# Kernel optimization log

Hardware: AMD Instinct MI355X
Metric: run time of the kernel (lower is better)

Reference implementation:

```python
import jax, jax.numpy as jnp
import numpy as np

H = 4  # num_heads


def transformer_conv(x, src, dst, wq, bq, wk, bk, wv, bv, ws, bs):
    # PyG TransformerConv, concat=False, root_weight=True, eval mode (no dropout).
    N = x.shape[0]
    C = wq.shape[1] // H  # per-head channels
    q = (x @ wq + bq).reshape(N, H, C)
    k = (x @ wk + bk).reshape(N, H, C)
    v = (x @ wv + bv).reshape(N, H, C)
    # per-edge attention logits: query at dst, key at src
    logits = (q[dst] * k[src]).sum(-1) / jnp.sqrt(jnp.asarray(C, x.dtype))  # [E,H]
    # scatter-softmax over incoming edges of each destination node
    m = jax.lax.stop_gradient(jax.ops.segment_max(logits, dst, num_segments=N))
    m = jnp.where(jnp.isfinite(m), m, jnp.zeros_like(m))
    e = jnp.exp(logits - m[dst])
    denom = jax.ops.segment_sum(e, dst, num_segments=N)
    alpha = e / (denom[dst] + 1e-16)  # [E,H]
    out = jax.ops.segment_sum(alpha[:, :, None] * v[src], dst, num_segments=N)  # [N,H,C]
    return out.mean(axis=1) + x @ ws + bs  # head-average + skip


def setup_inputs() -> dict:
    key = jax.random.key(0)
    ks = jax.random.split(key, 16)
    N, E, D, HID, OUT = 50000, 800000, 128, 32, 40
    s = 0.05
    inp = {
        "x": jax.random.normal(ks[0], (N, D), jnp.float32),
        "edge_index": jax.random.randint(ks[1], (2, E), 0, N, jnp.int64),
        "wq1": jax.random.normal(ks[2], (D, H * HID), jnp.float32) * s,
        "bq1": jnp.zeros((H * HID,), jnp.float32),
        "wk1": jax.random.normal(ks[3], (D, H * HID), jnp.float32) * s,
        "bk1": jnp.zeros((H * HID,), jnp.float32),
        "wv1": jax.random.normal(ks[4], (D, H * HID), jnp.float32) * s,
        "bv1": jnp.zeros((H * HID,), jnp.float32),
        "ws1": jax.random.normal(ks[5], (D, HID), jnp.float32) * s,
        "bs1": jnp.zeros((HID,), jnp.float32),
        "wq2": jax.random.normal(ks[6], (HID, H * HID), jnp.float32) * s,
        "bq2": jnp.zeros((H * HID,), jnp.float32),
        "wk2": jax.random.normal(ks[7], (HID, H * HID), jnp.float32) * s,
        "bk2": jnp.zeros((H * HID,), jnp.float32),
        "wv2": jax.random.normal(ks[8], (HID, H * HID), jnp.float32) * s,
        "bv2": jnp.zeros((H * HID,), jnp.float32),
        "ws2": jax.random.normal(ks[9], (HID, HID), jnp.float32) * s,
        "bs2": jnp.zeros((HID,), jnp.float32),
        "wc": jax.random.normal(ks[10], (HID, OUT), jnp.float32) * s,
        "bc": jnp.zeros((OUT,), jnp.float32),
    }
    return inp


def reference(x, edge_index, wq1, bq1, wk1, bk1, wv1, bv1, ws1, bs1,
              wq2, bq2, wk2, bk2, wv2, bv2, ws2, bs2, wc, bc):
    src, dst = edge_index[0], edge_index[1]
    h = jax.nn.relu(transformer_conv(x, src, dst, wq1, bq1, wk1, bk1, wv1, bv1, ws1, bs1))
    h = jax.nn.relu(transformer_conv(h, src, dst, wq2, bq2, wk2, bk2, wv2, bv2, ws2, bs2))
    return h @ wc + bc
```

## Files before the change

### kernel.cpp

```cpp
#include <hip/hip_runtime.h>
#include <hip/hip_bf16.h>

typedef __attribute__((ext_vector_type(8))) short short8;
typedef __attribute__((ext_vector_type(4))) float floatx4;
typedef __attribute__((ext_vector_type(4))) unsigned short ushort4v;

__device__ inline unsigned short f2bf(float x) {
    unsigned int u = __float_as_uint(x);
    u += 0x7FFFu + ((u >> 16) & 1u);
    return (unsigned short)(u >> 16);
}
__device__ inline float bf2f(unsigned short h) {
    return __uint_as_float(((unsigned int)h) << 16);
}
__device__ inline float blo(unsigned int u) { return __uint_as_float(u << 16); }
__device__ inline float bhi(unsigned int u) { return __uint_as_float(u & 0xFFFF0000u); }

#if defined(__has_builtin)
#if __has_builtin(__builtin_amdgcn_exp2f)
#define EXP2F(x) __builtin_amdgcn_exp2f(x)
#else
#define EXP2F(x) exp2f(x)
#endif
#if __has_builtin(__builtin_amdgcn_update_dpp)
#define HAVE_DPP 1
#endif
#else
#define EXP2F(x) exp2f(x)
#endif

#ifdef HAVE_DPP
template <int CTRL>
__device__ __forceinline__ float dppadd(float x) {
    int s = __builtin_amdgcn_update_dpp(0, __float_as_int(x), CTRL, 0xf, 0xf, true);
    return x + __int_as_float(s);
}
__device__ __forceinline__ float red8(float x) {
    x = dppadd<0xB1>(x);
    x = dppadd<0x4E>(x);
    x = dppadd<0x141>(x);
    return x;
}
__device__ __forceinline__ float xor8add(float x) {
    return dppadd<0x128>(x);
}
#else
__device__ __forceinline__ float red8(float x) {
    x += __shfl_xor(x, 1); x += __shfl_xor(x, 2); x += __shfl_xor(x, 4);
    return x;
}
__device__ __forceinline__ float xor8add(float x) { return x + __shfl_xor(x, 8); }
#endif

template <bool B> struct BC { static constexpr bool value = B; };

__global__ __launch_bounds__(256) void hist_kernel(
    const int* __restrict__ dst, int* __restrict__ deg, int E)
{
    int e = blockIdx.x * blockDim.x + threadIdx.x;
    if (e < E) atomicAdd(&deg[dst[e]], 1);
}

__global__ __launch_bounds__(256) void scan_part(
    const int* __restrict__ deg, int* __restrict__ bsum, int N)
{
    __shared__ int ws[4];
    const int base = blockIdx.x * 1024;
    const int tid = threadIdx.x, lane = tid & 63, w = tid >> 6;
    int s = 0;
#pragma unroll
    for (int j = 0; j < 4; j++) {
        int i = base + j * 256 + tid;
        if (i < N) s += deg[i];
    }
#pragma unroll
    for (int off = 1; off < 64; off <<= 1) s += __shfl_xor(s, off, 64);
    if (lane == 0) ws[w] = s;
    __syncthreads();
    if (tid == 0) bsum[blockIdx.x] = ws[0] + ws[1] + ws[2] + ws[3];
}

__global__ __launch_bounds__(64) void scan_tops(
    const int* __restrict__ bsum, int* __restrict__ boff,
    int* __restrict__ rowptr, int nb, int N)
{
    int lane = threadIdx.x;
    int v = (lane < nb) ? bsum[lane] : 0;
    int inc = v;
#pragma unroll
    for (int off = 1; off < 64; off <<= 1) {
        int t = __shfl_up(inc, off, 64);
        if (lane >= off) inc += t;
    }
    if (lane < nb) boff[lane] = inc - v;
    if (lane == 63) rowptr[N] = inc;
}

__global__ __launch_bounds__(256) void scan_final(
    const int* __restrict__ deg, const int* __restrict__ boff,
    int* __restrict__ rowptr, int* __restrict__ cursor, int N)
{
    __shared__ int woff[4];
    const int base = blockIdx.x * 1024;
    const int tid = threadIdx.x, lane = tid & 63, w = tid >> 6;
    const int i0 = base + tid * 4;
    int v0 = (i0     < N) ? deg[i0]     : 0;
    int v1 = (i0 + 1 < N) ? deg[i0 + 1] : 0;
    int v2 = (i0 + 2 < N) ? deg[i0 + 2] : 0;
    int v3 = (i0 + 3 < N) ? deg[i0 + 3] : 0;
    int ts = v0 + v1 + v2 + v3;
    int inc = ts;
#pragma unroll
    for (int off = 1; off < 64; off <<= 1) {
        int t = __shfl_up(inc, off, 64);
        if (lane >= off) inc += t;
    }
    if (lane == 63) woff[w] = inc;
    __syncthreads();
    int wpre = 0;
    if (w > 0) wpre += woff[0];
    if (w > 1) wpre += woff[1];
    if (w > 2) wpre += woff[2];
    int exc = boff[blockIdx.x] + wpre + inc - ts;
    int p0 = exc, p1 = exc + v0, p2 = p1 + v1, p3 = p2 + v2;
    if (i0     < N) { rowptr[i0]     = p0; cursor[i0]     = p0; }
    if (i0 + 1 < N) { rowptr[i0 + 1] = p1; cursor[i0 + 1] = p1; }
    if (i0 + 2 < N) { rowptr[i0 + 2] = p2; cursor[i0 + 2] = p2; }
    if (i0 + 3 < N) { rowptr[i0 + 3] = p3; cursor[i0 + 3] = p3; }
}

__global__ __launch_bounds__(256) void fill_kernel(
    const int* __restrict__ src, const int* __restrict__ dst,
    int* __restrict__ cursor, int* __restrict__ perm, int E)
{
    int e = blockIdx.x * blockDim.x + threadIdx.x;
    if (e >= E) return;
    int pos = atomicAdd(&cursor[dst[e]], 1);
    perm[pos] = src[e];
}

__global__ __launch_bounds__(128) void wprep_all(
    const float* __restrict__ wq1, const float* __restrict__ bq1,
    const float* __restrict__ wk1, const float* __restrict__ bk1,
    const float* __restrict__ wv1, const float* __restrict__ bv1,
    const float* __restrict__ ws1, const float* __restrict__ bs1,
    const float* __restrict__ wq2, const float* __restrict__ bq2,
    const float* __restrict__ wk2, const float* __restrict__ bk2,
    const float* __restrict__ wv2, const float* __restrict__ bv2,
    const float* __restrict__ ws2, const float* __restrict__ bs2,
    unsigned short* __restrict__ wt1h, unsigned short* __restrict__ wt1l,
    float* __restrict__ bias1,
    unsigned short* __restrict__ wt2h, unsigned short* __restrict__ wt2l,
    float* __restrict__ bias2,
    int* __restrict__ deg, int* __restrict__ perm, int N, int E)
{
    const int t = threadIdx.x;
    {
        int gid = blockIdx.x * 128 + t;
        if (gid < N) deg[gid] = 0;
        else if (gid < N + 48) perm[E + (gid - N)] = 0;
    }
    const int layer = (blockIdx.x >= 416) ? 1 : 0;
    const int c = blockIdx.x - layer * 416;
    const int L = layer ? 32 : 128;
    if (t >= L) return;
    const float* w; const float* b; int cc, ncols;
    if (c < 384) {
        int m = c >> 7; cc = c & 127; ncols = 128;
        if (layer == 0) {
            w = (m == 0) ? wq1 : ((m == 1) ? wk1 : wv1);
            b = (m == 0) ? bq1 : ((m == 1) ? bk1 : bv1);
        } else {
            w = (m == 0) ? wq2 : ((m == 1) ? wk2 : wv2);
            b = (m == 0) ? bq2 : ((m == 1) ? bk2 : bv2);
        }
    } else {
        cc = c - 384; ncols = 32;
        w = layer ? ws2 : ws1; b = layer ? bs2 : bs1;
    }
    unsigned short* wh = layer ? wt2h : wt1h;
    unsigned short* wl = layer ? wt2l : wt1l;
    float* bias = layer ? bias2 : bias1;
    const float QSCL = 0.17677669529663687f * 1.4426950408889634f;
    const float f = (c < 128) ? QSCL : 1.0f;
    float val = w[t * ncols + cc] * f;
    unsigned short h = f2bf(val);
    wh[c * L + t] = h;
    wl[c * L + t] = f2bf(val - bf2f(h));
    if (t == 0) bias[c] = b[cc] * f;
}

template <int L>
__global__ __launch_bounds__(512) void proj_mfma(
    const float* __restrict__ xin,
    const unsigned short* __restrict__ wt_hi,
    const unsigned short* __restrict__ wt_lo,
    const float* __restrict__ bias,
    float* __restrict__ q, unsigned short* __restrict__ kvp,
    float* __restrict__ skip, int N)
{
    constexpr int LP = L + 8;
    constexpr int KS = L / 32;
    constexpr int ELEMS = 32 * (L / 4);
    constexpr int SI = (ELEMS + 511) / 512;
    __shared__ unsigned short xh[2][32 * LP];
    __shared__ unsigned short xl[2][32 * LP];
    __shared__ float scr[8][32 * 36];
    const int tid = threadIdx.x, lane = tid & 63, w = tid >> 6;
    const int li = lane & 15, quad = lane >> 4;
    const int slot = __builtin_amdgcn_readfirstlane(blockIdx.y * 8 + w);
    const bool hasT = slot < 13;

    int t0 = 24, t1 = 25;
    if (slot < 4)       { t0 = slot * 2; t1 = t0 + 1; }
    else if (slot < 12) { t0 = 4 + slot; t1 = 12 + slot; }

    short8 Ah[2][KS], Al[2][KS];
    float bias_r[2][4];
    if (hasT) {
#pragma unroll
        for (int ti = 0; ti < 2; ti++) {
            int tt = ti ? t1 : t0;
#pragma unroll
            for (int ks = 0; ks < KS; ks++) {
                long off = (long)(tt * 16 + li) * L + ks * 32 + quad * 8;
                Ah[ti][ks] = *(const short8*)(wt_hi + off);
                Al[ti][ks] = *(const short8*)(wt_lo + off);
            }
#pragma unroll
            for (int r = 0; r < 4; r++)
                bias_r[ti][r] = bias[tt * 16 + quad * 4 + r];
        }
    }

    const int nb0 = blockIdx.x * 256;
    float* myscr = scr[w];
    unsigned int* su = (unsigned int*)myscr;

    float4 xv[SI];
    auto issue_loads = [&](int c) {
#pragma unroll
        for (int s = 0; s < SI; s++) {
            int f = s * 512 + tid;
            if (f < ELEMS) {
                int row = f / (L / 4), c4 = (f - row * (L / 4)) * 4;
                int n = nb0 + c * 32 + row;
                xv[s] = (n < N) ? *(const float4*)(xin + (long)n * L + c4)
                                : make_float4(0.f, 0.f, 0.f, 0.f);
            }
        }
    };
    auto cvt_store = [&](int buf) {
#pragma unroll
        for (int s = 0; s < SI; s++) {
            int f = s * 512 + tid;
            if (f < ELEMS) {
                int row = f / (L / 4), c4 = (f - row * (L / 4)) * 4;
                unsigned short h0 = f2bf(xv[s].x), h1 = f2bf(xv[s].y),
                               h2 = f2bf(xv[s].z), h3 = f2bf(xv[s].w);
                ushort4v hs = {h0, h1, h2, h3};
                ushort4v ls = {f2bf(xv[s].x - bf2f(h0)), f2bf(xv[s].y - bf2f(h1)),
                               f2bf(xv[s].z - bf2f(h2)), f2bf(xv[s].w - bf2f(h3))};
                *(ushort4v*)(xh[buf] + row * LP + c4) = hs;
                *(ushort4v*)(xl[buf] + row * LP + c4) = ls;
            }
        }
    };

    issue_loads(0);
    cvt_store(0);
    __syncthreads();

    for (int c = 0; c < 8; c++) {
        if (c < 7) issue_loads(c + 1);
        const int n0c = nb0 + c * 32;
        if (hasT) {
            const int buf = c & 1;
#pragma unroll
            for (int half = 0; half < 2; half++) {
                short8 Bh[KS], Bl[KS];
#pragma unroll
                for (int ks = 0; ks < KS; ks++) {
                    int off = (half * 16 + li) * LP + ks * 32 + quad * 8;
                    Bh[ks] = *(const short8*)(xh[buf] + off);
                    Bl[ks] = *(const short8*)(xl[buf] + off);
                }
                floatx4 accv[2];
#pragma unroll
                for (int ti = 0; ti < 2; ti++) {
                    floatx4 acc = {0.f, 0.f, 0.f, 0.f};
#pragma unroll
                    for (int ks = 0; ks < KS; ks++) {
                        acc = __builtin_amdgcn_mfma_f32_16x16x32_bf16(Ah[ti][ks], Bh[ks], acc, 0, 0, 0);
                        acc = __builtin_amdgcn_mfma_f32_16x16x32_bf16(Ah[ti][ks], Bl[ks], acc, 0, 0, 0);
                        acc = __builtin_amdgcn_mfma_f32_16x16x32_bf16(Al[ti][ks], Bh[ks], acc, 0, 0, 0);
                    }
#pragma unroll
                    for (int r = 0; r < 4; r++) acc[r] += bias_r[ti][r];
                    accv[ti] = acc;
                }
                const int row = half * 16 + li;
                if (slot < 4 || slot == 12) {
                    *(floatx4*)(myscr + row * 36 + quad * 4)      = accv[0];
                    *(floatx4*)(myscr + row * 36 + 16 + quad * 4) = accv[1];
                } else {
                    unsigned int k01 = (unsigned int)f2bf(accv[0][0]) | ((unsigned int)f2bf(accv[0][1]) << 16);
                    unsigned int k23 = (unsigned int)f2bf(accv[0][2]) | ((unsigned int)f2bf(accv[0][3]) << 16);
                    unsigned int v01 = (unsigned int)f2bf(accv[1][0]) | ((unsigned int)f2bf(accv[1][1]) << 16);
                    unsigned int v23 = (unsigned int)f2bf(accv[1][2]) | ((unsigned int)f2bf(accv[1][3]) << 16);
                    uint4 pk = make_uint4(k01, v01, k23, v23);
                    *(uint4*)(su + row * 20 + quad * 4) = pk;
                }
            }
            if (slot < 4) {
#pragma unroll
                for (int it = 0; it < 4; it++) {
                    int idx = it * 64 + lane;
                    int nl = idx >> 3, seg = idx & 7;
                    int node = n0c + nl;
                    if (node < N) {
                        floatx4 vv = *(floatx4*)(myscr + nl * 36 + seg * 4);
                        *(floatx4*)(q + (long)node * 128 + slot * 32 + seg * 4) = vv;
                    }
                }
            } else if (slot == 12) {
#pragma unroll
                for (int it = 0; it < 4; it++) {
                    int idx = it * 64 + lane;
                    int nl = idx >> 3, seg = idx & 7;
                    int node = n0c + nl;
                    if (node < N) {
                        floatx4 vv = *(floatx4*)(myscr + nl * 36 + seg * 4);
                        *(floatx4*)(skip + (long)node * 32 + seg * 4) = vv;
                    }
                }
            } else {
                const int i = slot - 4;
#pragma unroll
                for (int it = 0; it < 2; it++) {
                    int idx = it * 64 + lane;
                    int nl = idx >> 2, part = idx & 3;
                    int node = n0c + nl;
                    if (node < N) {
                        uint4 vv = *(uint4*)(su + nl * 20 + part * 4);
                        *(uint4*)((unsigned int*)(kvp + (long)node * 256) + i * 16 + part * 4) = vv;
                    }
                }
            }
        }
        __syncthreads();
        if (c < 7) cvt_store((c + 1) & 1);
        __syncthreads();
    }
}

template <bool FUSE_CLS>
__global__ __launch_bounds__(256) void attn_kernel(
    const float* __restrict__ q, const unsigned short* __restrict__ kvp,
    const int* __restrict__ rowptr, const int* __restrict__ perm,
    const float* __restrict__ skip, float* __restrict__ h,
    const float* __restrict__ wc, const float* __restrict__ bc,
    float* __restrict__ out, int N, int E)
{
    __shared__ float hrow[4][32];
    const int tid = threadIdx.x;
    const int wid = (blockIdx.x * 256 + tid) >> 6;
    const int wv = (tid >> 6) & 3;
    const int lane = tid & 63;
    if (wid >= N) return;
    const int d = __builtin_amdgcn_readfirstlane(wid);
    const int eh = lane >> 5;
    const int sl = lane & 31;
    const int hh = sl >> 3;
    const int g  = sl & 7;
    const unsigned dby = (unsigned)(hh * 64 + g * 8) * 2u;
    const char* __restrict__ kvb = (const char*)kvp;
    const float4 q4 = *(const float4*)(q + (long)d * 128 + hh * 32 + g * 4);

    const int beg = rowptr[d], end = rowptr[d + 1];
    const int n = end - beg;
    const int na = (n + 1) >> 1;
    const int nmin = n - na;
    const int my_off = beg + (eh ? na : 0);
    const int my_cnt = eh ? nmin : na;
    const int* __restrict__ pp = perm + my_off;

    float den = 0.f;
    float o0 = 0.f, o1 = 0.f, o2 = 0.f, o3 = 0.f;

    auto kvld = [&](int s) -> uint4 {
        return *(const uint4*)(kvb + ((((unsigned)s) << 9) + dby));
    };

    uint4 A0, A1, A2, A3, B0, B1, B2, B3, C0, C1, C2, C3;
    int PA0, PA1, PA2, PA3, PB0, PB1, PB2, PB3, PC0, PC1, PC2, PC3;
    {
        int i0 = pp[0], i1 = pp[1], i2  = pp[2],  i3  = pp[3];
        int i4 = pp[4], i5 = pp[5], i6  = pp[6],  i7  = pp[7];
        int i8 = pp[8], i9 = pp[9], i10 = pp[10], i11 = pp[11];
        PA0 = pp[12]; PA1 = pp[13]; PA2 = pp[14]; PA3 = pp[15];
        PB0 = pp[16]; PB1 = pp[17]; PB2 = pp[18]; PB3 = pp[19];
        PC0 = pp[20]; PC1 = pp[21]; PC2 = pp[22]; PC3 = pp[23];
        A0 = kvld(i0); A1 = kvld(i1); A2 = kvld(i2);  A3 = kvld(i3);
        B0 = kvld(i4); B1 = kvld(i5); B2 = kvld(i6);  B3 = kvld(i7);
        C0 = kvld(i8); C1 = kvld(i9); C2 = kvld(i10); C3 = kvld(i11);
    }

    auto grp = [&](const uint4& G0, const uint4& G1, const uint4& G2,
                   const uint4& G3, int jb, auto mc) {
        constexpr bool MASKED = decltype(mc)::value;
        float p0 = q4.x * blo(G0.x) + q4.y * bhi(G0.x) + q4.z * blo(G0.z) + q4.w * bhi(G0.z);
        float p1 = q4.x * blo(G1.x) + q4.y * bhi(G1.x) + q4.z * blo(G1.z) + q4.w * bhi(G1.z);
        float p2 = q4.x * blo(G2.x) + q4.y * bhi(G2.x) + q4.z * blo(G2.z) + q4.w * bhi(G2.z);
        float p3 = q4.x * blo(G3.x) + q4.y * bhi(G3.x) + q4.z * blo(G3.z) + q4.w * bhi(G3.z);
        p0 = red8(p0); p1 = red8(p1); p2 = red8(p2); p3 = red8(p3);
        p0 = fminf(p0, 60.f); p1 = fminf(p1, 60.f);
        p2 = fminf(p2, 60.f); p3 = fminf(p3, 60.f);
        if (MASKED) {
            p0 = (jb + 0 < my_cnt) ? p0 : -INFINITY;
            p1 = (jb + 1 < my_cnt) ? p1 : -INFINITY;
            p2 = (jb + 2 < my_cnt) ? p2 : -INFINITY;
            p3 = (jb + 3 < my_cnt) ? p3 : -INFINITY;
        }
        const float w0 = EXP2F(p0), w1 = EXP2F(p1);
        const float w2 = EXP2F(p2), w3 = EXP2F(p3);
        den += (w0 + w1) + (w2 + w3);
        o0 += w0 * blo(G0.y) + w1 * blo(G1.y) + w2 * blo(G2.y) + w3 * blo(G3.y);
        o1 += w0 * bhi(G0.y) + w1 * bhi(G1.y) + w2 * bhi(G2.y) + w3 * bhi(G3.y);
        o2 += w0 * blo(G0.w) + w1 * blo(G1.w) + w2 * blo(G2.w) + w3 * blo(G3.w);
        o3 += w0 * bhi(G0.w) + w1 * bhi(G1.w) + w2 * bhi(G2.w) + w3 * bhi(G3.w);
    };

    int j = 0;
    for (; j + 12 <= nmin; j += 12) {
        grp(A0, A1, A2, A3, j, BC<false>{});
        A0 = kvld(PA0); A1 = kvld(PA1); A2 = kvld(PA2); A3 = kvld(PA3);
        PA0 = pp[j + 24]; PA1 = pp[j + 25]; PA2 = pp[j + 26]; PA3 = pp[j + 27];
        grp(B0, B1, B2, B3, j + 4, BC<false>{});
        B0 = kvld(PB0); B1 = kvld(PB1); B2 = kvld(PB2); B3 = kvld(PB3);
        PB0 = pp[j + 28]; PB1 = pp[j + 29]; PB2 = pp[j + 30]; PB3 = pp[j + 31];
        grp(C0, C1, C2, C3, j + 8, BC<false>{});
        C0 = kvld(PC0); C1 = kvld(PC1); C2 = kvld(PC2); C3 = kvld(PC3);
        PC0 = pp[j + 32]; PC1 = pp[j + 33]; PC2 = pp[j + 34]; PC3 = pp[j + 35];
    }
    if (j < na) {
        grp(A0, A1, A2, A3, j, BC<true>{});
        if (j + 4 < na) grp(B0, B1, B2, B3, j + 4, BC<true>{});
        if (j + 8 < na) grp(C0, C1, C2, C3, j + 8, BC<true>{});
    }

    den += __shfl_xor(den, 32);
    o0 += __shfl_xor(o0, 32);
    o1 += __shfl_xor(o1, 32);
    o2 += __shfl_xor(o2, 32);
    o3 += __shfl_xor(o3, 32);

    const float inv = 1.f / (den + 1e-16f);
    o0 *= inv; o1 *= inv; o2 *= inv; o3 *= inv;
    o0 = xor8add(o0); o1 = xor8add(o1);
    o2 = xor8add(o2); o3 = xor8add(o3);
    o0 += __shfl_xor(o0, 16); o1 += __shfl_xor(o1, 16);
    o2 += __shfl_xor(o2, 16); o3 += __shfl_xor(o3, 16);

    if (lane < 8) {
        float4 sk = *(const float4*)(skip + (long)d * 32 + g * 4);
        float r0 = 0.25f * o0 + sk.x;
        float r1 = 0.25f * o1 + sk.y;
        float r2 = 0.25f * o2 + sk.z;
        float r3 = 0.25f * o3 + sk.w;
        r0 = r0 > 0.f ? r0 : 0.f;
        r1 = r1 > 0.f ? r1 : 0.f;
        r2 = r2 > 0.f ? r2 : 0.f;
        r3 = r3 > 0.f ? r3 : 0.f;
        if (FUSE_CLS) {
            *(float4*)&hrow[wv][g * 4] = make_float4(r0, r1, r2, r3);
        } else {
            *(float4*)(h + (long)d * 32 + g * 4) = make_float4(r0, r1, r2, r3);
        }
    }
    if (FUSE_CLS) {
        __builtin_amdgcn_wave_barrier();
        if (lane < 40) {
            float acc = bc[lane];
#pragma unroll
            for (int l = 0; l < 32; ++l)
                acc = fmaf(hrow[wv][l], wc[l * 40 + lane], acc);
            out[(long)d * 40 + lane] = acc;
        }
    }
}

extern "C" void kernel_launch(void* const* d_in, const int* in_sizes, int n_in,
                              void* d_out, int out_size, void* d_ws, size_t ws_size,
                              hipStream_t stream)
{
    const float* x   = (const float*)d_in[0];
    const int* ei    = (const int*)d_in[1];
    const float* wq1 = (const float*)d_in[2];  const float* bq1 = (const float*)d_in[3];
    const float* wk1 = (const float*)d_in[4];  const float* bk1 = (const float*)d_in[5];
    const float* wv1 = (const float*)d_in[6];  const float* bv1 = (const float*)d_in[7];
    const float* ws1 = (const float*)d_in[8];  const float* bs1 = (const float*)d_in[9];
    const float* wq2 = (const float*)d_in[10]; const float* bq2 = (const float*)d_in[11];
    const float* wk2 = (const float*)d_in[12]; const float* bk2 = (const float*)d_in[13];
    const float* wv2 = (const float*)d_in[14]; const float* bv2 = (const float*)d_in[15];
    const float* ws2 = (const float*)d_in[16]; const float* bs2 = (const float*)d_in[17];
    const float* wc  = (const float*)d_in[18]; const float* bc  = (const float*)d_in[19];

    const int N = in_sizes[0] / 128;
    const int E = in_sizes[1] / 2;
    const int* src = ei;
    const int* dst = ei + E;

    char* p = (char*)d_ws;
    auto take = [&](size_t bytes) { char* r = p; p += (bytes + 255) & ~(size_t)255; return r; };
    float* q             = (float*)take((size_t)N * 128 * 4);
    unsigned short* kvp  = (unsigned short*)take((size_t)N * 256 * 2);
    float* skip          = (float*)take((size_t)N * 32 * 4);
    float* h1            = (float*)take((size_t)N * 32 * 4);
    unsigned short* wt1h = (unsigned short*)take(416 * 128 * 2);
    unsigned short* wt1l = (unsigned short*)take(416 * 128 * 2);
    unsigned short* wt2h = (unsigned short*)take(416 * 32 * 2);
    unsigned short* wt2l = (unsigned short*)take(416 * 32 * 2);
    float* bias1         = (float*)take(416 * 4);
    float* bias2         = (float*)take(416 * 4);
    int* deg             = (int*)take((size_t)N * 4);
    int* rowptr          = (int*)take((size_t)(N + 1) * 4);
    int* cursor          = (int*)take((size_t)N * 4);
    int* perm            = (int*)take((size_t)(E + 48) * 4);
    int* bsum            = (int*)take(64 * 4);
    int* boff            = (int*)take(64 * 4);

    const dim3 projGrid((N + 255) / 256, 2);
    const int eGrid    = (E + 255) / 256;
    const int attnGrid = (N + 3) / 4;
    const int nb       = (N + 1023) / 1024;

    wprep_all<<<832, 128, 0, stream>>>(wq1, bq1, wk1, bk1, wv1, bv1, ws1, bs1,
                                       wq2, bq2, wk2, bk2, wv2, bv2, ws2, bs2,
                                       wt1h, wt1l, bias1, wt2h, wt2l, bias2,
                                       deg, perm, N, E);
    hist_kernel<<<eGrid, 256, 0, stream>>>(dst, deg, E);
    scan_part<<<nb, 256, 0, stream>>>(deg, bsum, N);
    scan_tops<<<1, 64, 0, stream>>>(bsum, boff, rowptr, nb, N);
    scan_final<<<nb, 256, 0, stream>>>(deg, boff, rowptr, cursor, N);
    fill_kernel<<<eGrid, 256, 0, stream>>>(src, dst, cursor, perm, E);

    proj_mfma<128><<<projGrid, 512, 0, stream>>>(x, wt1h, wt1l, bias1, q, kvp, skip, N);
    attn_kernel<false><<<attnGrid, 256, 0, stream>>>(q, kvp, rowptr, perm, skip, h1,
                                                     wc, bc, (float*)d_out, N, E);

    proj_mfma<32><<<projGrid, 512, 0, stream>>>(h1, wt2h, wt2l, bias2, q, kvp, skip, N);
    attn_kernel<true><<<attnGrid, 256, 0, stream>>>(q, kvp, rowptr, perm, skip, h1,
                                                    wc, bc, (float*)d_out, N, E);
}
```

Baseline: 366.3 us.

## Fuse weight prep with histogram and layer-1 projection with CSR fill

Merges the weight-prep kernel and the degree histogram into a single launch that splits work by block index. The layer-1 projection and the CSR fill kernel are merged the same way, so the atomic scatter overlaps with the MFMA projection. Zeroing of deg moves to hipMemsetAsync and the perm padding moves into scan_tops. The aim is to cut launch count and let independent work share the GPU, at the cost of a larger heterogeneous grid whose fill blocks reserve the projection's shared memory.

```diff
diff --git a/kernel.cpp b/kernel.cpp
--- a/kernel.cpp
+++ b/kernel.cpp
@@ -54,11 +54,56 @@
 
 template <bool B> struct BC { static constexpr bool value = B; };
 
-__global__ __launch_bounds__(256) void hist_kernel(
+__global__ __launch_bounds__(256) void wprep_hist(
+    const float* __restrict__ wq1, const float* __restrict__ bq1,
+    const float* __restrict__ wk1, const float* __restrict__ bk1,
+    const float* __restrict__ wv1, const float* __restrict__ bv1,
+    const float* __restrict__ ws1, const float* __restrict__ bs1,
+    const float* __restrict__ wq2, const float* __restrict__ bq2,
+    const float* __restrict__ wk2, const float* __restrict__ bk2,
+    const float* __restrict__ wv2, const float* __restrict__ bv2,
+    const float* __restrict__ ws2, const float* __restrict__ bs2,
+    unsigned short* __restrict__ wt1h, unsigned short* __restrict__ wt1l,
+    float* __restrict__ bias1,
+    unsigned short* __restrict__ wt2h, unsigned short* __restrict__ wt2l,
+    float* __restrict__ bias2,
     const int* __restrict__ dst, int* __restrict__ deg, int E)
 {
-    int e = blockIdx.x * blockDim.x + threadIdx.x;
-    if (e < E) atomicAdd(&deg[dst[e]], 1);
+    const int bx = blockIdx.x;
+    const int t = threadIdx.x;
+    if (bx >= 832) {
+        int e = (bx - 832) * 256 + t;
+        if (e < E) atomicAdd(&deg[dst[e]], 1);
+        return;
+    }
+    const int layer = (bx >= 416) ? 1 : 0;
+    const int c = bx - layer * 416;
+    const int L = layer ? 32 : 128;
+    if (t >= L) return;
+    const float* w; const float* b; int cc, ncols;
+    if (c < 384) {
+        int m = c >> 7; cc = c & 127; ncols = 128;
+        if (layer == 0) {
+            w = (m == 0) ? wq1 : ((m == 1) ? wk1 : wv1);
+            b = (m == 0) ? bq1 : ((m == 1) ? bk1 : bv1);
+        } else {
+            w = (m == 0) ? wq2 : ((m == 1) ? wk2 : wv2);
+            b = (m == 0) ? bq2 : ((m == 1) ? bk2 : bv2);
+        }
+    } else {
+        cc = c - 384; ncols = 32;
+        w = layer ? ws2 : ws1; b = layer ? bs2 : bs1;
+    }
+    unsigned short* wh = layer ? wt2h : wt1h;
+    unsigned short* wl = layer ? wt2l : wt1l;
+    float* bias = layer ? bias2 : bias1;
+    const float QSCL = 0.17677669529663687f * 1.4426950408889634f;
+    const float f = (c < 128) ? QSCL : 1.0f;
+    float val = w[t * ncols + cc] * f;
+    unsigned short h = f2bf(val);
+    wh[c * L + t] = h;
+    wl[c * L + t] = f2bf(val - bf2f(h));
+    if (t == 0) bias[c] = b[cc] * f;
 }
 
 __global__ __launch_bounds__(256) void scan_part(
@@ -82,9 +127,11 @@
 
 __global__ __launch_bounds__(64) void scan_tops(
     const int* __restrict__ bsum, int* __restrict__ boff,
-    int* __restrict__ rowptr, int nb, int N)
+    int* __restrict__ rowptr, int nb, int N,
+    int* __restrict__ perm, int E)
 {
     int lane = threadIdx.x;
+    if (lane < 48) perm[E + lane] = 0;
     int v = (lane < nb) ? bsum[lane] : 0;
     int inc = v;
 #pragma unroll
@@ -129,65 +176,182 @@
     if (i0 + 3 < N) { rowptr[i0 + 3] = p3; cursor[i0 + 3] = p3; }
 }
 
-__global__ __launch_bounds__(256) void fill_kernel(
+__global__ __launch_bounds__(512) void proj1_fill(
+    const float* __restrict__ xin,
+    const unsigned short* __restrict__ wt_hi,
+    const unsigned short* __restrict__ wt_lo,
+    const float* __restrict__ bias,
+    float* __restrict__ q, unsigned short* __restrict__ kvp,
+    float* __restrict__ skip, int N, int projNB,
     const int* __restrict__ src, const int* __restrict__ dst,
     int* __restrict__ cursor, int* __restrict__ perm, int E)
 {
-    int e = blockIdx.x * blockDim.x + threadIdx.x;
-    if (e >= E) return;
-    int pos = atomicAdd(&cursor[dst[e]], 1);
-    perm[pos] = src[e];
-}
-
-__global__ __launch_bounds__(128) void wprep_all(
-    const float* __restrict__ wq1, const float* __restrict__ bq1,
-    const float* __restrict__ wk1, const float* __restrict__ bk1,
-    const float* __restrict__ wv1, const float* __restrict__ bv1,
-    const float* __restrict__ ws1, const float* __restrict__ bs1,
-    const float* __restrict__ wq2, const float* __restrict__ bq2,
-    const float* __restrict__ wk2, const float* __restrict__ bk2,
-    const float* __restrict__ wv2, const float* __restrict__ bv2,
-    const float* __restrict__ ws2, const float* __restrict__ bs2,
-    unsigned short* __restrict__ wt1h, unsigned short* __restrict__ wt1l,
-    float* __restrict__ bias1,
-    unsigned short* __restrict__ wt2h, unsigned short* __restrict__ wt2l,
-    float* __restrict__ bias2,
-    int* __restrict__ deg, int* __restrict__ perm, int N, int E)
-{
-    const int t = threadIdx.x;
-    {
-        int gid = blockIdx.x * 128 + t;
-        if (gid < N) deg[gid] = 0;
-        else if (gid < N + 48) perm[E + (gid - N)] = 0;
-    }
-    const int layer = (blockIdx.x >= 416) ? 1 : 0;
-    const int c = blockIdx.x - layer * 416;
-    const int L = layer ? 32 : 128;
-    if (t >= L) return;
-    const float* w; const float* b; int cc, ncols;
-    if (c < 384) {
-        int m = c >> 7; cc = c & 127; ncols = 128;
-        if (layer == 0) {
-            w = (m == 0) ? wq1 : ((m == 1) ? wk1 : wv1);
-            b = (m == 0) ? bq1 : ((m == 1) ? bk1 : bv1);
-        } else {
-            w = (m == 0) ? wq2 : ((m == 1) ? wk2 : wv2);
-            b = (m == 0) ? bq2 : ((m == 1) ? bk2 : bv2);
-        }
-    } else {
-        cc = c - 384; ncols = 32;
-        w = layer ? ws2 : ws1; b = layer ? bs2 : bs1;
-    }
-    unsigned short* wh = layer ? wt2h : wt1h;
-    unsigned short* wl = layer ? wt2l : wt1l;
-    float* bias = layer ? bias2 : bias1;
-    const float QSCL = 0.17677669529663687f * 1.4426950408889634f;
-    const float f = (c < 128) ? QSCL : 1.0f;
-    float val = w[t * ncols + cc] * f;
-    unsigned short h = f2bf(val);
-    wh[c * L + t] = h;
-    wl[c * L + t] = f2bf(val - bf2f(h));
-    if (t == 0) bias[c] = b[cc] * f;
+    constexpr int L = 128;
+    constexpr int LP = L + 8;
+    constexpr int KS = L / 32;
+    constexpr int ELEMS = 32 * (L / 4);
+    constexpr int SI = (ELEMS + 511) / 512;
+    __shared__ unsigned short xh[2][32 * LP];
+    __shared__ unsigned short xl[2][32 * LP];
+    __shared__ float scr[8][32 * 36];
+
+    const int bx = blockIdx.x;
+    const int tid = threadIdx.x;
+    if (bx >= projNB * 2) {
+        int e = (bx - projNB * 2) * 512 + tid;
+        if (e < E) {
+            int pos = atomicAdd(&cursor[dst[e]], 1);
+            perm[pos] = src[e];
+        }
+        return;
+    }
+
+    const int lane = tid & 63, w = tid >> 6;
+    const int li = lane & 15, quad = lane >> 4;
+    const int slot = __builtin_amdgcn_readfirstlane((bx & 1) * 8 + w);
+    const bool hasT = slot < 13;
+
+    int t0 = 24, t1 = 25;
+    if (slot < 4)       { t0 = slot * 2; t1 = t0 + 1; }
+    else if (slot < 12) { t0 = 4 + slot; t1 = 12 + slot; }
+
+    short8 Ah[2][KS], Al[2][KS];
+    float bias_r[2][4];
+    if (hasT) {
+#pragma unroll
+        for (int ti = 0; ti < 2; ti++) {
+            int tt = ti ? t1 : t0;
+#pragma unroll
+            for (int ks = 0; ks < KS; ks++) {
+                long off = (long)(tt * 16 + li) * L + ks * 32 + quad * 8;
+                Ah[ti][ks] = *(const short8*)(wt_hi + off);
+                Al[ti][ks] = *(const short8*)(wt_lo + off);
+            }
+#pragma unroll
+            for (int r = 0; r < 4; r++)
+                bias_r[ti][r] = bias[tt * 16 + quad * 4 + r];
+        }
+    }
+
+    const int nb0 = (bx >> 1) * 256;
+    float* myscr = scr[w];
+    unsigned int* su = (unsigned int*)myscr;
+
+    float4 xv[SI];
+    auto issue_loads = [&](int c) {
+#pragma unroll
+        for (int s = 0; s < SI; s++) {
+            int f = s * 512 + tid;
+            if (f < ELEMS) {
+                int row = f / (L / 4), c4 = (f - row * (L / 4)) * 4;
+                int n = nb0 + c * 32 + row;
+                xv[s] = (n < N) ? *(const float4*)(xin + (long)n * L + c4)
+                                : make_float4(0.f, 0.f, 0.f, 0.f);
+            }
+        }
+    };
+    auto cvt_store = [&](int buf) {
+#pragma unroll
+        for (int s = 0; s < SI; s++) {
+            int f = s * 512 + tid;
+            if (f < ELEMS) {
+                int row = f / (L / 4), c4 = (f - row * (L / 4)) * 4;
+                unsigned short h0 = f2bf(xv[s].x), h1 = f2bf(xv[s].y),
+                               h2 = f2bf(xv[s].z), h3 = f2bf(xv[s].w);
+                ushort4v hs = {h0, h1, h2, h3};
+                ushort4v ls = {f2bf(xv[s].x - bf2f(h0)), f2bf(xv[s].y - bf2f(h1)),
+                               f2bf(xv[s].z - bf2f(h2)), f2bf(xv[s].w - bf2f(h3))};
+                *(ushort4v*)(xh[buf] + row * LP + c4) = hs;
+                *(ushort4v*)(xl[buf] + row * LP + c4) = ls;
+            }
+        }
+    };
+
+    issue_loads(0);
+    cvt_store(0);
+    __syncthreads();
+
+    for (int c = 0; c < 8; c++) {
+        if (c < 7) issue_loads(c + 1);
+        const int n0c = nb0 + c * 32;
+        if (hasT) {
+            const int buf = c & 1;
+#pragma unroll
+            for (int half = 0; half < 2; half++) {
+                short8 Bh[KS], Bl[KS];
+#pragma unroll
+                for (int ks = 0; ks < KS; ks++) {
+                    int off = (half * 16 + li) * LP + ks * 32 + quad * 8;
+                    Bh[ks] = *(const short8*)(xh[buf] + off);
+                    Bl[ks] = *(const short8*)(xl[buf] + off);
+                }
+                floatx4 accv[2];
+#pragma unroll
+                for (int ti = 0; ti < 2; ti++) {
+                    floatx4 acc = {0.f, 0.f, 0.f, 0.f};
+#pragma unroll
+                    for (int ks = 0; ks < KS; ks++) {
+                        acc = __builtin_amdgcn_mfma_f32_16x16x32_bf16(Ah[ti][ks], Bh[ks], acc, 0, 0, 0);
+                        acc = __builtin_amdgcn_mfma_f32_16x16x32_bf16(Ah[ti][ks], Bl[ks], acc, 0, 0, 0);
+                        acc = __builtin_amdgcn_mfma_f32_16x16x32_bf16(Al[ti][ks], Bh[ks], acc, 0, 0, 0);
+                    }
+#pragma unroll
+                    for (int r = 0; r < 4; r++) acc[r] += bias_r[ti][r];
+                    accv[ti] = acc;
+                }
+                const int row = half * 16 + li;
+                if (slot < 4 || slot == 12) {
+                    *(floatx4*)(myscr + row * 36 + quad * 4)      = accv[0];
+                    *(floatx4*)(myscr + row * 36 + 16 + quad * 4) = accv[1];
+                } else {
+                    unsigned int k01 = (unsigned int)f2bf(accv[0][0]) | ((unsigned int)f2bf(accv[0][1]) << 16);
+                    unsigned int k23 = (unsigned int)f2bf(accv[0][2]) | ((unsigned int)f2bf(accv[0][3]) << 16);
+                    unsigned int v01 = (unsigned int)f2bf(accv[1][0]) | ((unsigned int)f2bf(accv[1][1]) << 16);
+                    unsigned int v23 = (unsigned int)f2bf(accv[1][2]) | ((unsigned int)f2bf(accv[1][3]) << 16);
+                    uint4 pk = make_uint4(k01, v01, k23, v23);
+                    *(uint4*)(su + row * 20 + quad * 4) = pk;
+                }
+            }
+            if (slot < 4) {
+#pragma unroll
+                for (int it = 0; it < 4; it++) {
+                    int idx = it * 64 + lane;
+                    int nl = idx >> 3, seg = idx & 7;
+                    int node = n0c + nl;
+                    if (node < N) {
+                        floatx4 vv = *(floatx4*)(myscr + nl * 36 + seg * 4);
+                        *(floatx4*)(q + (long)node * 128 + slot * 32 + seg * 4) = vv;
+                    }
+                }
+            } else if (slot == 12) {
+#pragma unroll
+                for (int it = 0; it < 4; it++) {
+                    int idx = it * 64 + lane;
+                    int nl = idx >> 3, seg = idx & 7;
+                    int node = n0c + nl;
+                    if (node < N) {
+                        floatx4 vv = *(floatx4*)(myscr + nl * 36 + seg * 4);
+                        *(floatx4*)(skip + (long)node * 32 + seg * 4) = vv;
+                    }
+                }
+            } else {
+                const int i = slot - 4;
+#pragma unroll
+                for (int it = 0; it < 2; it++) {
+                    int idx = it * 64 + lane;
+                    int nl = idx >> 2, part = idx & 3;
+                    int node = n0c + nl;
+                    if (node < N) {
+                        uint4 vv = *(uint4*)(su + nl * 20 + part * 4);
+                        *(uint4*)((unsigned int*)(kvp + (long)node * 256) + i * 16 + part * 4) = vv;
+                    }
+                }
+            }
+        }
+        __syncthreads();
+        if (c < 7) cvt_store((c + 1) & 1);
+        __syncthreads();
+    }
 }
 
 template <int L>
@@ -530,26 +694,30 @@
     int* bsum            = (int*)take(64 * 4);
     int* boff            = (int*)take(64 * 4);
 
-    const dim3 projGrid((N + 255) / 256, 2);
-    const int eGrid    = (E + 255) / 256;
+    const int projNB   = (N + 255) / 256;
+    const int eGrid256 = (E + 255) / 256;
+    const int eGrid512 = (E + 511) / 512;
     const int attnGrid = (N + 3) / 4;
     const int nb       = (N + 1023) / 1024;
 
-    wprep_all<<<832, 128, 0, stream>>>(wq1, bq1, wk1, bk1, wv1, bv1, ws1, bs1,
-                                       wq2, bq2, wk2, bk2, wv2, bv2, ws2, bs2,
-                                       wt1h, wt1l, bias1, wt2h, wt2l, bias2,
-                                       deg, perm, N, E);
-    hist_kernel<<<eGrid, 256, 0, stream>>>(dst, deg, E);
+    hipMemsetAsync(deg, 0, (size_t)N * 4, stream);
+    wprep_hist<<<832 + eGrid256, 256, 0, stream>>>(
+        wq1, bq1, wk1, bk1, wv1, bv1, ws1, bs1,
+        wq2, bq2, wk2, bk2, wv2, bv2, ws2, bs2,
+        wt1h, wt1l, bias1, wt2h, wt2l, bias2,
+        dst, deg, E);
     scan_part<<<nb, 256, 0, stream>>>(deg, bsum, N);
-    scan_tops<<<1, 64, 0, stream>>>(bsum, boff, rowptr, nb, N);
+    scan_tops<<<1, 64, 0, stream>>>(bsum, boff, rowptr, nb, N, perm, E);
     scan_final<<<nb, 256, 0, stream>>>(deg, boff, rowptr, cursor, N);
-    fill_kernel<<<eGrid, 256, 0, stream>>>(src, dst, cursor, perm, E);
-
-    proj_mfma<128><<<projGrid, 512, 0, stream>>>(x, wt1h, wt1l, bias1, q, kvp, skip, N);
+
+    proj1_fill<<<projNB * 2 + eGrid512, 512, 0, stream>>>(
+        x, wt1h, wt1l, bias1, q, kvp, skip, N, projNB,
+        src, dst, cursor, perm, E);
     attn_kernel<false><<<attnGrid, 256, 0, stream>>>(q, kvp, rowptr, perm, skip, h1,
                                                      wc, bc, (float*)d_out, N, E);
 
-    proj_mfma<32><<<projGrid, 512, 0, stream>>>(h1, wt2h, wt2l, bias2, q, kvp, skip, N);
+    proj_mfma<32><<<dim3(projNB, 2), 512, 0, stream>>>(h1, wt2h, wt2l, bias2,
+                                                       q, kvp, skip, N);
     attn_kernel<true><<<attnGrid, 256, 0, stream>>>(q, kvp, rowptr, perm, skip, h1,
                                                     wc, bc, (float*)d_out, N, E);
 }
```

After: 350.7 us, median of 2. 1.04x faster.

## Fuse CSR fill into projection launch and weight prep into histogram

Applied to the files above, without the earlier changes.

Merges the weight-prep kernel with the degree histogram and the CSR fill kernel with the layer-1 projection, using extra blocks in each launch, so the launch count drops and independent work can overlap. The degree buffer is now cleared with a memset, and the perm padding is zeroed in scan_tops. The projection tile shrinks from 256 to 128 nodes per block, and the scratch staging is halved by writing out each 16-row half right after it is computed. This doubles the block count and cuts shared memory, at the cost of more per-block weight-fragment loads.

```diff
diff --git a/kernel.cpp b/kernel.cpp
--- a/kernel.cpp
+++ b/kernel.cpp
@@ -54,11 +54,56 @@
 
 template <bool B> struct BC { static constexpr bool value = B; };
 
-__global__ __launch_bounds__(256) void hist_kernel(
+__global__ __launch_bounds__(256) void wprep_hist(
+    const float* __restrict__ wq1, const float* __restrict__ bq1,
+    const float* __restrict__ wk1, const float* __restrict__ bk1,
+    const float* __restrict__ wv1, const float* __restrict__ bv1,
+    const float* __restrict__ ws1, const float* __restrict__ bs1,
+    const float* __restrict__ wq2, const float* __restrict__ bq2,
+    const float* __restrict__ wk2, const float* __restrict__ bk2,
+    const float* __restrict__ wv2, const float* __restrict__ bv2,
+    const float* __restrict__ ws2, const float* __restrict__ bs2,
+    unsigned short* __restrict__ wt1h, unsigned short* __restrict__ wt1l,
+    float* __restrict__ bias1,
+    unsigned short* __restrict__ wt2h, unsigned short* __restrict__ wt2l,
+    float* __restrict__ bias2,
     const int* __restrict__ dst, int* __restrict__ deg, int E)
 {
-    int e = blockIdx.x * blockDim.x + threadIdx.x;
-    if (e < E) atomicAdd(&deg[dst[e]], 1);
+    const int bx = blockIdx.x;
+    const int t = threadIdx.x;
+    if (bx >= 832) {
+        int e = (bx - 832) * 256 + t;
+        if (e < E) atomicAdd(&deg[dst[e]], 1);
+        return;
+    }
+    const int layer = (bx >= 416) ? 1 : 0;
+    const int c = bx - layer * 416;
+    const int L = layer ? 32 : 128;
+    if (t >= L) return;
+    const float* w; const float* b; int cc, ncols;
+    if (c < 384) {
+        int m = c >> 7; cc = c & 127; ncols = 128;
+        if (layer == 0) {
+            w = (m == 0) ? wq1 : ((m == 1) ? wk1 : wv1);
+            b = (m == 0) ? bq1 : ((m == 1) ? bk1 : bv1);
+        } else {
+            w = (m == 0) ? wq2 : ((m == 1) ? wk2 : wv2);
+            b = (m == 0) ? bq2 : ((m == 1) ? bk2 : bv2);
+        }
+    } else {
+        cc = c - 384; ncols = 32;
+        w = layer ? ws2 : ws1; b = layer ? bs2 : bs1;
+    }
+    unsigned short* wh = layer ? wt2h : wt1h;
+    unsigned short* wl = layer ? wt2l : wt1l;
+    float* bias = layer ? bias2 : bias1;
+    const float QSCL = 0.17677669529663687f * 1.4426950408889634f;
+    const float f = (c < 128) ? QSCL : 1.0f;
+    float val = w[t * ncols + cc] * f;
+    unsigned short h = f2bf(val);
+    wh[c * L + t] = h;
+    wl[c * L + t] = f2bf(val - bf2f(h));
+    if (t == 0) bias[c] = b[cc] * f;
 }
 
 __global__ __launch_bounds__(256) void scan_part(
@@ -82,9 +127,11 @@
 
 __global__ __launch_bounds__(64) void scan_tops(
     const int* __restrict__ bsum, int* __restrict__ boff,
-    int* __restrict__ rowptr, int nb, int N)
+    int* __restrict__ rowptr, int nb, int N,
+    int* __restrict__ perm, int E)
 {
     int lane = threadIdx.x;
+    if (lane < 48) perm[E + lane] = 0;
     int v = (lane < nb) ? bsum[lane] : 0;
     int inc = v;
 #pragma unroll
@@ -129,86 +176,40 @@
     if (i0 + 3 < N) { rowptr[i0 + 3] = p3; cursor[i0 + 3] = p3; }
 }
 
-__global__ __launch_bounds__(256) void fill_kernel(
-    const int* __restrict__ src, const int* __restrict__ dst,
-    int* __restrict__ cursor, int* __restrict__ perm, int E)
-{
-    int e = blockIdx.x * blockDim.x + threadIdx.x;
-    if (e >= E) return;
-    int pos = atomicAdd(&cursor[dst[e]], 1);
-    perm[pos] = src[e];
-}
-
-__global__ __launch_bounds__(128) void wprep_all(
-    const float* __restrict__ wq1, const float* __restrict__ bq1,
-    const float* __restrict__ wk1, const float* __restrict__ bk1,
-    const float* __restrict__ wv1, const float* __restrict__ bv1,
-    const float* __restrict__ ws1, const float* __restrict__ bs1,
-    const float* __restrict__ wq2, const float* __restrict__ bq2,
-    const float* __restrict__ wk2, const float* __restrict__ bk2,
-    const float* __restrict__ wv2, const float* __restrict__ bv2,
-    const float* __restrict__ ws2, const float* __restrict__ bs2,
-    unsigned short* __restrict__ wt1h, unsigned short* __restrict__ wt1l,
-    float* __restrict__ bias1,
-    unsigned short* __restrict__ wt2h, unsigned short* __restrict__ wt2l,
-    float* __restrict__ bias2,
-    int* __restrict__ deg, int* __restrict__ perm, int N, int E)
-{
-    const int t = threadIdx.x;
-    {
-        int gid = blockIdx.x * 128 + t;
-        if (gid < N) deg[gid] = 0;
-        else if (gid < N + 48) perm[E + (gid - N)] = 0;
-    }
-    const int layer = (blockIdx.x >= 416) ? 1 : 0;
-    const int c = blockIdx.x - layer * 416;
-    const int L = layer ? 32 : 128;
-    if (t >= L) return;
-    const float* w; const float* b; int cc, ncols;
-    if (c < 384) {
-        int m = c >> 7; cc = c & 127; ncols = 128;
-        if (layer == 0) {
-            w = (m == 0) ? wq1 : ((m == 1) ? wk1 : wv1);
-            b = (m == 0) ? bq1 : ((m == 1) ? bk1 : bv1);
-        } else {
-            w = (m == 0) ? wq2 : ((m == 1) ? wk2 : wv2);
-            b = (m == 0) ? bq2 : ((m == 1) ? bk2 : bv2);
-        }
-    } else {
-        cc = c - 384; ncols = 32;
-        w = layer ? ws2 : ws1; b = layer ? bs2 : bs1;
-    }
-    unsigned short* wh = layer ? wt2h : wt1h;
-    unsigned short* wl = layer ? wt2l : wt1l;
-    float* bias = layer ? bias2 : bias1;
-    const float QSCL = 0.17677669529663687f * 1.4426950408889634f;
-    const float f = (c < 128) ? QSCL : 1.0f;
-    float val = w[t * ncols + cc] * f;
-    unsigned short h = f2bf(val);
-    wh[c * L + t] = h;
-    wl[c * L + t] = f2bf(val - bf2f(h));
-    if (t == 0) bias[c] = b[cc] * f;
-}
-
 template <int L>
-__global__ __launch_bounds__(512) void proj_mfma(
+__global__ __launch_bounds__(512) void proj_fused(
     const float* __restrict__ xin,
     const unsigned short* __restrict__ wt_hi,
     const unsigned short* __restrict__ wt_lo,
     const float* __restrict__ bias,
     float* __restrict__ q, unsigned short* __restrict__ kvp,
-    float* __restrict__ skip, int N)
+    float* __restrict__ skip, int N, int projNB2,
+    const int* __restrict__ src, const int* __restrict__ dst,
+    int* __restrict__ cursor, int* __restrict__ perm, int E)
 {
     constexpr int LP = L + 8;
     constexpr int KS = L / 32;
+    constexpr int CI = 4;
     constexpr int ELEMS = 32 * (L / 4);
     constexpr int SI = (ELEMS + 511) / 512;
     __shared__ unsigned short xh[2][32 * LP];
     __shared__ unsigned short xl[2][32 * LP];
-    __shared__ float scr[8][32 * 36];
-    const int tid = threadIdx.x, lane = tid & 63, w = tid >> 6;
+    __shared__ float scr[8][16 * 36];
+
+    const int bx = blockIdx.x;
+    const int tid = threadIdx.x;
+    if (bx >= projNB2) {
+        int e = (bx - projNB2) * 512 + tid;
+        if (e < E) {
+            int pos = atomicAdd(&cursor[dst[e]], 1);
+            perm[pos] = src[e];
+        }
+        return;
+    }
+
+    const int lane = tid & 63, w = tid >> 6;
     const int li = lane & 15, quad = lane >> 4;
-    const int slot = __builtin_amdgcn_readfirstlane(blockIdx.y * 8 + w);
+    const int slot = __builtin_amdgcn_readfirstlane((bx & 1) * 8 + w);
     const bool hasT = slot < 13;
 
     int t0 = 24, t1 = 25;
@@ -233,7 +234,7 @@
         }
     }
 
-    const int nb0 = blockIdx.x * 256;
+    const int nb0 = (bx >> 1) * 128;
     float* myscr = scr[w];
     unsigned int* su = (unsigned int*)myscr;
 
@@ -271,8 +272,8 @@
     cvt_store(0);
     __syncthreads();
 
-    for (int c = 0; c < 8; c++) {
-        if (c < 7) issue_loads(c + 1);
+    for (int c = 0; c < CI; c++) {
+        if (c < CI - 1) issue_loads(c + 1);
         const int n0c = nb0 + c * 32;
         if (hasT) {
             const int buf = c & 1;
@@ -299,57 +300,55 @@
                     for (int r = 0; r < 4; r++) acc[r] += bias_r[ti][r];
                     accv[ti] = acc;
                 }
-                const int row = half * 16 + li;
                 if (slot < 4 || slot == 12) {
-                    *(floatx4*)(myscr + row * 36 + quad * 4)      = accv[0];
-                    *(floatx4*)(myscr + row * 36 + 16 + quad * 4) = accv[1];
+                    *(floatx4*)(myscr + li * 36 + quad * 4)      = accv[0];
+                    *(floatx4*)(myscr + li * 36 + 16 + quad * 4) = accv[1];
                 } else {
                     unsigned int k01 = (unsigned int)f2bf(accv[0][0]) | ((unsigned int)f2bf(accv[0][1]) << 16);
                     unsigned int k23 = (unsigned int)f2bf(accv[0][2]) | ((unsigned int)f2bf(accv[0][3]) << 16);
                     unsigned int v01 = (unsigned int)f2bf(accv[1][0]) | ((unsigned int)f2bf(accv[1][1]) << 16);
                     unsigned int v23 = (unsigned int)f2bf(accv[1][2]) | ((unsigned int)f2bf(accv[1][3]) << 16);
                     uint4 pk = make_uint4(k01, v01, k23, v23);
-                    *(uint4*)(su + row * 20 + quad * 4) = pk;
+                    *(uint4*)(su + li * 20 + quad * 4) = pk;
                 }
-            }
-            if (slot < 4) {
-#pragma unroll
-                for (int it = 0; it < 4; it++) {
-                    int idx = it * 64 + lane;
-                    int nl = idx >> 3, seg = idx & 7;
-                    int node = n0c + nl;
-                    if (node < N) {
-                        floatx4 vv = *(floatx4*)(myscr + nl * 36 + seg * 4);
-                        *(floatx4*)(q + (long)node * 128 + slot * 32 + seg * 4) = vv;
+                __builtin_amdgcn_wave_barrier();
+                const int nbh = n0c + half * 16;
+                if (slot < 4) {
+#pragma unroll
+                    for (int it = 0; it < 2; it++) {
+                        int idx = it * 64 + lane;
+                        int nl = idx >> 3, seg = idx & 7;
+                        int node = nbh + nl;
+                        if (node < N) {
+                            floatx4 vv = *(floatx4*)(myscr + nl * 36 + seg * 4);
+                            *(floatx4*)(q + (long)node * 128 + slot * 32 + seg * 4) = vv;
+                        }
                     }
-                }
-            } else if (slot == 12) {
-#pragma unroll
-                for (int it = 0; it < 4; it++) {
-                    int idx = it * 64 + lane;
-                    int nl = idx >> 3, seg = idx & 7;
-                    int node = n0c + nl;
-                    if (node < N) {
-                        floatx4 vv = *(floatx4*)(myscr + nl * 36 + seg * 4);
-                        *(floatx4*)(skip + (long)node * 32 + seg * 4) = vv;
+                } else if (slot == 12) {
+#pragma unroll
+                    for (int it = 0; it < 2; it++) {
+                        int idx = it * 64 + lane;
+                        int nl = idx >> 3, seg = idx & 7;
+                        int node = nbh + nl;
+                        if (node < N) {
+                            floatx4 vv = *(floatx4*)(myscr + nl * 36 + seg * 4);
+                            *(floatx4*)(skip + (long)node * 32 + seg * 4) = vv;
+                        }
                     }
-                }
-            } else {
-                const int i = slot - 4;
-#pragma unroll
-                for (int it = 0; it < 2; it++) {
-                    int idx = it * 64 + lane;
-                    int nl = idx >> 2, part = idx & 3;
-                    int node = n0c + nl;
+                } else {
+                    const int i = slot - 4;
+                    int nl = lane >> 2, part = lane & 3;
+                    int node = nbh + nl;
                     if (node < N) {
                         uint4 vv = *(uint4*)(su + nl * 20 + part * 4);
                         *(uint4*)((unsigned int*)(kvp + (long)node * 256) + i * 16 + part * 4) = vv;
                     }
                 }
+                __builtin_amdgcn_wave_barrier();
             }
         }
         __syncthreads();
-        if (c < 7) cvt_store((c + 1) & 1);
+        if (c < CI - 1) cvt_store((c + 1) & 1);
         __syncthreads();
     }
 }
@@ -530,26 +529,32 @@
     int* bsum            = (int*)take(64 * 4);
     int* boff            = (int*)take(64 * 4);
 
-    const dim3 projGrid((N + 255) / 256, 2);
-    const int eGrid    = (E + 255) / 256;
+    const int projT    = (N + 127) / 128;
+    const int projNB2  = projT * 2;
+    const int eGrid256 = (E + 255) / 256;
+    const int eGrid512 = (E + 511) / 512;
     const int attnGrid = (N + 3) / 4;
     const int nb       = (N + 1023) / 1024;
 
-    wprep_all<<<832, 128, 0, stream>>>(wq1, bq1, wk1, bk1, wv1, bv1, ws1, bs1,
-                                       wq2, bq2, wk2, bk2, wv2, bv2, ws2, bs2,
-                                       wt1h, wt1l, bias1, wt2h, wt2l, bias2,
-                                       deg, perm, N, E);
-    hist_kernel<<<eGrid, 256, 0, stream>>>(dst, deg, E);
+    hipMemsetAsync(deg, 0, (size_t)N * 4, stream);
+    wprep_hist<<<832 + eGrid256, 256, 0, stream>>>(
+        wq1, bq1, wk1, bk1, wv1, bv1, ws1, bs1,
+        wq2, bq2, wk2, bk2, wv2, bv2, ws2, bs2,
+        wt1h, wt1l, bias1, wt2h, wt2l, bias2,
+        dst, deg, E);
     scan_part<<<nb, 256, 0, stream>>>(deg, bsum, N);
-    scan_tops<<<1, 64, 0, stream>>>(bsum, boff, rowptr, nb, N);
+    scan_tops<<<1, 64, 0, stream>>>(bsum, boff, rowptr, nb, N, perm, E);
     scan_final<<<nb, 256, 0, stream>>>(deg, boff, rowptr, cursor, N);
-    fill_kernel<<<eGrid, 256, 0, stream>>>(src, dst, cursor, perm, E);
-
-    proj_mfma<128><<<projGrid, 512, 0, stream>>>(x, wt1h, wt1l, bias1, q, kvp, skip, N);
+
+    proj_fused<128><<<projNB2 + eGrid512, 512, 0, stream>>>(
+        x, wt1h, wt1l, bias1, q, kvp, skip, N, projNB2,
+        src, dst, cursor, perm, E);
     attn_kernel<false><<<attnGrid, 256, 0, stream>>>(q, kvp, rowptr, perm, skip, h1,
                                                      wc, bc, (float*)d_out, N, E);
 
-    proj_mfma<32><<<projGrid, 512, 0, stream>>>(h1, wt2h, wt2l, bias2, q, kvp, skip, N);
+    proj_fused<32><<<projNB2, 512, 0, stream>>>(
+        h1, wt2h, wt2l, bias2, q, kvp, skip, N, projNB2,
+        src, dst, cursor, perm, 0);
     attn_kernel<true><<<attnGrid, 256, 0, stream>>>(q, kvp, rowptr, perm, skip, h1,
                                                     wc, bc, (float*)d_out, N, E);
 }
```

After: 367.5 us. About the same (+0.3%).
